# Kernel tuning notes

Measured on AMD Instinct MI355X. Metric: run time of the kernel, lower is better.

The kernel has to match this reference:

```python
import jax, jax.numpy as jnp
import numpy as np

HEADS = 16
D_MODEL = 1024
D_K = D_MODEL // HEADS
SEQ = 2048
BSZ = 2


def softmax_one(x, axis):
    # softmax with an extra +1 in the denominator ("attention off" slot)
    x = x - jnp.max(x, axis=axis, keepdims=True)
    ex = jnp.exp(x)
    return ex / (1.0 + jnp.sum(ex, axis=axis, keepdims=True))


def setup_inputs() -> dict:
    key = jax.random.key(0)
    ks = jax.random.split(key, 7)
    s = 1.0 / np.sqrt(D_MODEL)
    return {
        "x": jax.random.normal(ks[0], (SEQ, BSZ, D_MODEL), dtype=jnp.float32),
        "Wq": jax.random.normal(ks[1], (D_MODEL, D_MODEL), dtype=jnp.float32) * s,
        "bq": jnp.zeros((D_MODEL,), dtype=jnp.float32),
        "Wk": jax.random.normal(ks[2], (D_MODEL, D_MODEL), dtype=jnp.float32) * s,
        "bk": jnp.zeros((D_MODEL,), dtype=jnp.float32),
        "Wv": jax.random.normal(ks[3], (D_MODEL, D_MODEL), dtype=jnp.float32) * s,
        "bv": jnp.zeros((D_MODEL,), dtype=jnp.float32),
    }


def reference(x, Wq, bq, Wk, bk, Wv, bv):
    S, B, D = x.shape
    q = (x @ Wq.T + bq).reshape(S, B, HEADS, D_K)
    k = (x @ Wk.T + bk).reshape(S, B, HEADS, D_K)
    v = (x @ Wv.T + bv).reshape(S, B, HEADS, D_K)
    # [i, j, b, h] full score tensor, scaled by sqrt(d_k)
    scores = jnp.einsum('ibhd,jbhd->ijbh', q, k) / np.sqrt(D_K).astype(np.float32)
    causal = jnp.tril(jnp.ones((S, S), dtype=bool))[:, :, None, None]
    scores = jnp.where(causal, scores, -jnp.inf)
    attn = softmax_one(scores, axis=1)  # softmax over key axis j with +1 denom
    out = jnp.einsum('ijbh,jbhd->ibhd', attn, v)
    return out.reshape(S, B, D)
```

## Files before the change

### kernel.cpp

```cpp
#include <hip/hip_runtime.h>

#define SEQ 2048
#define BSZ 2
#define NH 16
#define DKD 64
#define DM 1024
#define NROW (SEQ*BSZ)
#define KDIM 1024
#define BIAS 16.0f

typedef __attribute__((ext_vector_type(8))) short bf16x8;
typedef __attribute__((ext_vector_type(4))) short bf16x4;
typedef __attribute__((ext_vector_type(4))) float floatx4;
typedef __attribute__((ext_vector_type(2))) unsigned uint2v;

__device__ __forceinline__ unsigned short f2b(float f) {
  unsigned int u = __builtin_bit_cast(unsigned int, f);
  u += 0x7fffu + ((u >> 16) & 1u);
  return (unsigned short)(u >> 16);
}

__device__ __forceinline__ void async_copy16(void* lds, const void* g) {
  __builtin_amdgcn_global_load_lds(
      (__attribute__((address_space(1))) void*)(void*)g,
      (__attribute__((address_space(3))) void*)lds, 16, 0, 0);
}

__device__ __forceinline__ floatx4 mfma16(bf16x8 a, bf16x8 b, floatx4 c) {
  return __builtin_amdgcn_mfma_f32_16x16x32_bf16(a, b, c, 0, 0, 0);
}

__device__ __forceinline__ floatx4 mfma16k(bf16x4 a, bf16x4 b, floatx4 c) {
#if __has_builtin(__builtin_amdgcn_mfma_f32_16x16x16bf16_1k)
  return __builtin_amdgcn_mfma_f32_16x16x16bf16_1k(a, b, c, 0, 0, 0);
#else
  floatx4 d;
  asm volatile("v_mfma_f32_16x16x16_bf16 %0, %1, %2, %3"
               : "=v"(d) : "v"(a), "v"(b), "v"(c));
  return d;
#endif
}

__global__ __launch_bounds__(256) void cvt_kernel(
    const float* __restrict__ x, const float* __restrict__ Wq,
    const float* __restrict__ Wk, const float* __restrict__ Wv,
    ushort* __restrict__ xbf, ushort* __restrict__ wbf) {
  size_t tid = (size_t)blockIdx.x * 256 + threadIdx.x;
  size_t i4 = tid * 4;
  const float* src;
  const size_t NX = (size_t)NROW * KDIM;
  ushort* dst;
  size_t off;
  if (i4 < NX) {
    src = x; off = i4; dst = xbf + i4;
  } else {
    size_t wix = i4 - NX;
    int proj = (int)(wix >> 20);
    src = proj == 0 ? Wq : (proj == 1 ? Wk : Wv);
    off = wix & 1048575u;
    dst = wbf + wix;
  }
  float4 v = *(const float4*)(src + off);
  ushort4 o;
  o.x = f2b(v.x); o.y = f2b(v.y); o.z = f2b(v.z); o.w = f2b(v.w);
  *(ushort4*)dst = o;
}

union GemmSmem {
  struct { ushort Al[128 * 32]; ushort Bl[128 * 32]; } ab;
  ushort Cl[128 * 136];
};

__global__ __launch_bounds__(256, 3) void gemm_qkv(
    const ushort* __restrict__ xbf, const ushort* __restrict__ wbf,
    const float* __restrict__ bq, const float* __restrict__ bk,
    const float* __restrict__ bvv,
    ushort* __restrict__ Qs, ushort* __restrict__ Ks, ushort* __restrict__ Vt) {
  __shared__ GemmSmem sm;
  const int t = threadIdx.x;
  const int w = t >> 6, l = t & 63;
  const int wr = w >> 1, wc = w & 1;
  const int lane15 = l & 15, quad = l >> 4;
  const int rb = blockIdx.x, cb = blockIdx.y;
  const ushort* Ag = xbf + (size_t)rb * 128 * KDIM;
  const ushort* Bg = wbf + (size_t)cb * 128 * KDIM;
  const int rsub = l >> 2, c2 = (l & 3) * 8;

  floatx4 acc[4][4];
  #pragma unroll
  for (int i = 0; i < 4; ++i)
    #pragma unroll
    for (int j = 0; j < 4; ++j) acc[i][j] = (floatx4){0.f, 0.f, 0.f, 0.f};

  for (int kk = 0; kk < KDIM; kk += 32) {
    __syncthreads();
    #pragma unroll
    for (int half = 0; half < 2; ++half) {
      int rloc = w * 32 + half * 16;
      async_copy16(&sm.ab.Al[rloc * 32], Ag + (size_t)(rloc + rsub) * KDIM + kk + c2);
      async_copy16(&sm.ab.Bl[rloc * 32], Bg + (size_t)(rloc + rsub) * KDIM + kk + c2);
    }
    __syncthreads();
    bf16x8 af[4], bfr[4];
    #pragma unroll
    for (int mt = 0; mt < 4; ++mt)
      af[mt] = *(const bf16x8*)&sm.ab.Al[(wr * 64 + mt * 16 + lane15) * 32 + quad * 8];
    #pragma unroll
    for (int nt = 0; nt < 4; ++nt)
      bfr[nt] = *(const bf16x8*)&sm.ab.Bl[(wc * 64 + nt * 16 + lane15) * 32 + quad * 8];
    #pragma unroll
    for (int mt = 0; mt < 4; ++mt)
      #pragma unroll
      for (int nt = 0; nt < 4; ++nt)
        acc[mt][nt] = mfma16(af[mt], bfr[nt], acc[mt][nt]);
  }
  __syncthreads();

  int proj = (cb * 128) >> 10;
  const float* bias = proj == 0 ? bq : (proj == 1 ? bk : bvv);
  float scale = proj == 0 ? 0.125f * 1.44269504088896f : 1.0f;
  bool isV = (proj == 2);

  #pragma unroll
  for (int nt = 0; nt < 4; ++nt) {
    int c = wc * 64 + nt * 16 + lane15;
    int cip = (cb * 128 + c) & 1023;
    float bias_v = bias[cip];
    #pragma unroll
    for (int mt = 0; mt < 4; ++mt) {
      #pragma unroll
      for (int r = 0; r < 4; ++r) {
        int n = wr * 64 + mt * 16 + quad * 4 + r;
        float val = (acc[mt][nt][r] + bias_v) * scale;
        if (!isV) sm.Cl[n * 136 + c] = f2b(val);
        else      sm.Cl[c * 136 + (n & 1) * 64 + (n >> 1)] = f2b(val);
      }
    }
  }
  __syncthreads();

  if (!isV) {
    ushort* dst = proj == 0 ? Qs : Ks;
    int b = t >> 7;
    int sl = t & 63;
    int chunk = (t >> 6) & 1;
    int n = (sl << 1) | b;
    int cip = (cb * 128 + chunk * 64) & 1023;
    int h = cip >> 6;
    int s = rb * 64 + sl;
    ushort* g = dst + (((size_t)(b * NH + h) * SEQ + s) * DKD);
    const uint4* s4 = (const uint4*)&sm.Cl[n * 136 + chunk * 64];
    #pragma unroll
    for (int j = 0; j < 8; ++j) *(uint4*)(g + j * 8) = s4[j];
  } else {
    int c = t >> 1, b = t & 1;
    int cip = (cb * 128 + c) & 1023;
    int h = cip >> 6, dk = c & 63;
    ushort* g = Vt + ((size_t)(b * NH + h) * DKD + dk) * SEQ + rb * 64;
    const uint4* s4 = (const uint4*)&sm.Cl[c * 136 + b * 64];
    #pragma unroll
    for (int j = 0; j < 8; ++j) *(uint4*)(g + j * 8) = s4[j];
  }
}

__global__ __launch_bounds__(256, 2) void attn_kernel(
    const ushort* __restrict__ Qs, const ushort* __restrict__ Ks,
    const ushort* __restrict__ Vt, float* __restrict__ out) {
  __shared__ ushort Kl[2][64 * 72];
  __shared__ ushort Vl[2][64 * 72];
  const int t = threadIdx.x;
  const int w = t >> 6, l = t & 63;
  const int lane15 = l & 15, quad = l >> 4;
  const int bh = blockIdx.x;
  const int qa = blockIdx.y;
  const int b = bh >> 4, h = bh & 15;

  const ushort* Kg = Ks + (size_t)bh * SEQ * DKD;
  const ushort* Vg = Vt + (size_t)bh * DKD * SEQ;
  const int srow = t >> 3;
  const int scol = (t & 7) * 8;

  int qt = qa;
  int qbase = qt * 64;
  const ushort* Qg = Qs + ((size_t)bh * SEQ + qbase + w * 16 + lane15) * DKD;
  bf16x8 qf0 = *(const bf16x8*)(Qg + quad * 8);
  bf16x8 qf1 = *(const bf16x8*)(Qg + 32 + quad * 8);

  floatx4 o[4];
  #pragma unroll
  for (int i = 0; i < 4; ++i) o[i] = (floatx4){0.f, 0.f, 0.f, 0.f};
  floatx4 lacc = (floatx4){0.f, 0.f, 0.f, 0.f};
  float pm = -1e30f;

  bf16x4 ones4;
  #pragma unroll
  for (int j = 0; j < 4; ++j) ones4[j] = (short)0x3F80;

  #define KT_OF(j) ((j) <= qa ? (j) : (j) - qa - 1)

  uint4 kr0, kr1, vr0, vr1;
  {
    kr0 = *(const uint4*)(Kg + (size_t)srow * DKD + scol);
    kr1 = *(const uint4*)(Kg + (size_t)(srow + 32) * DKD + scol);
    vr0 = *(const uint4*)(Vg + (size_t)srow * SEQ + scol);
    vr1 = *(const uint4*)(Vg + (size_t)(srow + 32) * SEQ + scol);
    *(uint4*)&Kl[0][srow * 72 + scol] = kr0;
    *(uint4*)&Kl[0][(srow + 32) * 72 + scol] = kr1;
    *(uint4*)&Vl[0][srow * 72 + scol] = vr0;
    *(uint4*)&Vl[0][(srow + 32) * 72 + scol] = vr1;
    int kt1 = KT_OF(1);
    kr0 = *(const uint4*)(Kg + (size_t)(kt1 * 64 + srow) * DKD + scol);
    kr1 = *(const uint4*)(Kg + (size_t)(kt1 * 64 + srow + 32) * DKD + scol);
    vr0 = *(const uint4*)(Vg + (size_t)srow * SEQ + kt1 * 64 + scol);
    vr1 = *(const uint4*)(Vg + (size_t)(srow + 32) * SEQ + kt1 * 64 + scol);
  }

  for (int it = 0; it <= 32; ++it) {
    const int cur = it & 1;
    const int kt = KT_OF(it);
    __syncthreads();

    floatx4 sf[4];
    #pragma unroll
    for (int nt = 0; nt < 4; ++nt) {
      floatx4 a = (floatx4){-BIAS, -BIAS, -BIAS, -BIAS};
      bf16x8 k0 = *(const bf16x8*)&Kl[cur][(nt * 16 + lane15) * 72 + quad * 8];
      bf16x8 k1 = *(const bf16x8*)&Kl[cur][(nt * 16 + lane15) * 72 + 32 + quad * 8];
      a = mfma16(k0, qf0, a);
      a = mfma16(k1, qf1, a);
      sf[nt] = a;
    }

    if (kt == qt) {
      int q_abs = qbase + w * 16 + lane15;
      #pragma unroll
      for (int nt = 0; nt < 4; ++nt) {
        #pragma unroll
        for (int r = 0; r < 4; ++r) {
          int k_abs = kt * 64 + nt * 16 + quad * 4 + r;
          if (k_abs > q_abs) sf[nt][r] = -1e30f;
        }
      }
    }

    bf16x4 pa[4];
    #pragma unroll
    for (int nt = 0; nt < 4; ++nt) {
      float p0 = __builtin_amdgcn_exp2f(sf[nt][0]);
      float p1 = __builtin_amdgcn_exp2f(sf[nt][1]);
      float p2 = __builtin_amdgcn_exp2f(sf[nt][2]);
      float p3 = __builtin_amdgcn_exp2f(sf[nt][3]);
      pm = fmaxf(pm, fmaxf(fmaxf(sf[nt][0], sf[nt][1]),
                           fmaxf(sf[nt][2], sf[nt][3])));
      unsigned u0 = __builtin_bit_cast(unsigned, p0);
      unsigned u1 = __builtin_bit_cast(unsigned, p1);
      unsigned u2 = __builtin_bit_cast(unsigned, p2);
      unsigned u3 = __builtin_bit_cast(unsigned, p3);
      uint2v pk;
      pk[0] = (u0 >> 16) | (u1 & 0xffff0000u);
      pk[1] = (u2 >> 16) | (u3 & 0xffff0000u);
      pa[nt] = __builtin_bit_cast(bf16x4, pk);
    }

    #pragma unroll
    for (int nt = 0; nt < 4; ++nt) lacc = mfma16k(pa[nt], ones4, lacc);
    #pragma unroll
    for (int ntd = 0; ntd < 4; ++ntd) {
      #pragma unroll
      for (int nt = 0; nt < 4; ++nt) {
        bf16x4 vf = *(const bf16x4*)&Vl[cur][(ntd * 16 + lane15) * 72 +
                                            nt * 16 + quad * 4];
        o[ntd] = mfma16k(pa[nt], vf, o[ntd]);
      }
    }

    if (it == qa || it == 32) {
      float pmr = fmaxf(pm, __shfl_xor(pm, 16, 64));
      pmr = fmaxf(pmr, __shfl_xor(pmr, 32, 64));
      float inv_[4];
      #pragma unroll
      for (int r = 0; r < 4; ++r) {
        float mq = __shfl(pmr, quad * 4 + r, 64);
        inv_[r] = 1.0f / (__builtin_amdgcn_exp2f(mq) + lacc[r]);
      }
      #pragma unroll
      for (int ntd = 0; ntd < 4; ++ntd) {
        int d = h * DKD + ntd * 16 + lane15;
        #pragma unroll
        for (int r = 0; r < 4; ++r) {
          int i = qbase + w * 16 + quad * 4 + r;
          out[((size_t)i * BSZ + b) * DM + d] = o[ntd][r] * inv_[r];
        }
      }
      if (it == qa) {
        #pragma unroll
        for (int i = 0; i < 4; ++i) o[i] = (floatx4){0.f, 0.f, 0.f, 0.f};
        lacc = (floatx4){0.f, 0.f, 0.f, 0.f};
        pm = -1e30f;
        qt = 31 - qa;
        qbase = qt * 64;
        const ushort* Qg2 = Qs + ((size_t)bh * SEQ + qbase + w * 16 + lane15) * DKD;
        qf0 = *(const bf16x8*)(Qg2 + quad * 8);
        qf1 = *(const bf16x8*)(Qg2 + 32 + quad * 8);
      }
    }

    if (it < 32) {
      int nxt = cur ^ 1;
      *(uint4*)&Kl[nxt][srow * 72 + scol] = kr0;
      *(uint4*)&Kl[nxt][(srow + 32) * 72 + scol] = kr1;
      *(uint4*)&Vl[nxt][srow * 72 + scol] = vr0;
      *(uint4*)&Vl[nxt][(srow + 32) * 72 + scol] = vr1;
      if (it + 2 <= 32) {
        int kt2 = KT_OF(it + 2);
        kr0 = *(const uint4*)(Kg + (size_t)(kt2 * 64 + srow) * DKD + scol);
        kr1 = *(const uint4*)(Kg + (size_t)(kt2 * 64 + srow + 32) * DKD + scol);
        vr0 = *(const uint4*)(Vg + (size_t)srow * SEQ + kt2 * 64 + scol);
        vr1 = *(const uint4*)(Vg + (size_t)(srow + 32) * SEQ + kt2 * 64 + scol);
      }
    }
  }
  #undef KT_OF
}

extern "C" void kernel_launch(void* const* d_in, const int* in_sizes, int n_in,
                              void* d_out, int out_size, void* d_ws, size_t ws_size,
                              hipStream_t stream) {
  (void)in_sizes; (void)n_in; (void)out_size; (void)ws_size;
  const float* x  = (const float*)d_in[0];
  const float* Wq = (const float*)d_in[1];
  const float* bq = (const float*)d_in[2];
  const float* Wk = (const float*)d_in[3];
  const float* bk = (const float*)d_in[4];
  const float* Wv = (const float*)d_in[5];
  const float* bv = (const float*)d_in[6];
  float* out = (float*)d_out;

  ushort* xbf = (ushort*)d_out;
  ushort* wbf = (ushort*)((char*)d_out + 8388608);

  char* ws = (char*)d_ws;
  ushort* Qs = (ushort*)(ws);
  ushort* Ks = (ushort*)(ws + 8388608);
  ushort* Vt = (ushort*)(ws + 16777216);

  cvt_kernel<<<dim3(7168), dim3(256), 0, stream>>>(x, Wq, Wk, Wv, xbf, wbf);
  gemm_qkv<<<dim3(32, 24), dim3(256), 0, stream>>>(xbf, wbf, bq, bk, bv, Qs, Ks, Vt);
  attn_kernel<<<dim3(32, 16), dim3(256), 0, stream>>>(Qs, Ks, Vt, out);
}
```

Baseline: 162.8 us.

## Double GEMM K-step with swizzled LDS and use 128-key tiles in attention

The QKV GEMM now stages 64-wide K slices per iteration, with an XOR swizzle on the LDS layout, so it needs half as many barriers and avoids bank conflicts on the fragment reads. The attention kernel loads 128-key K/V tiles per iteration, halving the loop count and its barriers, and skips the upper 64-key half on diagonal tiles. Each paired query tile now runs against 17 iterations of 128 keys instead of 33 of 64. LDS use roughly doubles in both kernels, which could lower occupancy, and the staged registers per thread also double.

```diff
diff --git a/kernel.cpp b/kernel.cpp
--- a/kernel.cpp
+++ b/kernel.cpp
@@ -67,7 +67,7 @@
 }
 
 union GemmSmem {
-  struct { ushort Al[128 * 32]; ushort Bl[128 * 32]; } ab;
+  struct { ushort Al[128 * 64]; ushort Bl[128 * 64]; } ab;
   ushort Cl[128 * 136];
 };
 
@@ -84,7 +84,8 @@
   const int rb = blockIdx.x, cb = blockIdx.y;
   const ushort* Ag = xbf + (size_t)rb * 128 * KDIM;
   const ushort* Bg = wbf + (size_t)cb * 128 * KDIM;
-  const int rsub = l >> 2, c2 = (l & 3) * 8;
+  const int srsub = l >> 3;
+  const int sgc = ((l & 7) ^ (l >> 3)) * 8;
 
   floatx4 acc[4][4];
   #pragma unroll
@@ -92,27 +93,40 @@
     #pragma unroll
     for (int j = 0; j < 4; ++j) acc[i][j] = (floatx4){0.f, 0.f, 0.f, 0.f};
 
-  for (int kk = 0; kk < KDIM; kk += 32) {
+  const int swzA = (lane15 & 7);
+
+  for (int kk = 0; kk < KDIM; kk += 64) {
     __syncthreads();
     #pragma unroll
-    for (int half = 0; half < 2; ++half) {
-      int rloc = w * 32 + half * 16;
-      async_copy16(&sm.ab.Al[rloc * 32], Ag + (size_t)(rloc + rsub) * KDIM + kk + c2);
-      async_copy16(&sm.ab.Bl[rloc * 32], Bg + (size_t)(rloc + rsub) * KDIM + kk + c2);
+    for (int c = 0; c < 4; ++c) {
+      int rloc = c * 32 + w * 8;
+      async_copy16(&sm.ab.Al[rloc * 64],
+                   Ag + (size_t)(rloc + srsub) * KDIM + kk + sgc);
+      async_copy16(&sm.ab.Bl[rloc * 64],
+                   Bg + (size_t)(rloc + srsub) * KDIM + kk + sgc);
     }
     __syncthreads();
-    bf16x8 af[4], bfr[4];
-    #pragma unroll
-    for (int mt = 0; mt < 4; ++mt)
-      af[mt] = *(const bf16x8*)&sm.ab.Al[(wr * 64 + mt * 16 + lane15) * 32 + quad * 8];
-    #pragma unroll
-    for (int nt = 0; nt < 4; ++nt)
-      bfr[nt] = *(const bf16x8*)&sm.ab.Bl[(wc * 64 + nt * 16 + lane15) * 32 + quad * 8];
-    #pragma unroll
-    for (int mt = 0; mt < 4; ++mt)
-      #pragma unroll
-      for (int nt = 0; nt < 4; ++nt)
-        acc[mt][nt] = mfma16(af[mt], bfr[nt], acc[mt][nt]);
+    #pragma unroll
+    for (int ks = 0; ks < 2; ++ks) {
+      bf16x8 af[4], bfr[4];
+      #pragma unroll
+      for (int mt = 0; mt < 4; ++mt) {
+        int row = wr * 64 + mt * 16 + lane15;
+        int pos = ((quad + ks * 4) ^ swzA) * 8;
+        af[mt] = *(const bf16x8*)&sm.ab.Al[row * 64 + pos];
+      }
+      #pragma unroll
+      for (int nt = 0; nt < 4; ++nt) {
+        int row = wc * 64 + nt * 16 + lane15;
+        int pos = ((quad + ks * 4) ^ swzA) * 8;
+        bfr[nt] = *(const bf16x8*)&sm.ab.Bl[row * 64 + pos];
+      }
+      #pragma unroll
+      for (int mt = 0; mt < 4; ++mt)
+        #pragma unroll
+        for (int nt = 0; nt < 4; ++nt)
+          acc[mt][nt] = mfma16(af[mt], bfr[nt], acc[mt][nt]);
+    }
   }
   __syncthreads();
 
@@ -166,19 +180,22 @@
 __global__ __launch_bounds__(256, 2) void attn_kernel(
     const ushort* __restrict__ Qs, const ushort* __restrict__ Ks,
     const ushort* __restrict__ Vt, float* __restrict__ out) {
-  __shared__ ushort Kl[2][64 * 72];
-  __shared__ ushort Vl[2][64 * 72];
+  __shared__ ushort Kl[2][128 * 72];
+  __shared__ ushort Vl[2][64 * 136];
   const int t = threadIdx.x;
   const int w = t >> 6, l = t & 63;
   const int lane15 = l & 15, quad = l >> 4;
   const int bh = blockIdx.x;
   const int qa = blockIdx.y;
   const int b = bh >> 4, h = bh & 15;
+  const int lastA = qa >> 1;
 
   const ushort* Kg = Ks + (size_t)bh * SEQ * DKD;
   const ushort* Vg = Vt + (size_t)bh * DKD * SEQ;
-  const int srow = t >> 3;
-  const int scol = (t & 7) * 8;
+  const int krow = t >> 3;
+  const int kcol = (t & 7) * 8;
+  const int vrow = t >> 4;
+  const int vcol = (t & 15) * 8;
 
   int qt = qa;
   int qbase = qt * 64;
@@ -196,85 +213,93 @@
   #pragma unroll
   for (int j = 0; j < 4; ++j) ones4[j] = (short)0x3F80;
 
-  #define KT_OF(j) ((j) <= qa ? (j) : (j) - qa - 1)
-
-  uint4 kr0, kr1, vr0, vr1;
-  {
-    kr0 = *(const uint4*)(Kg + (size_t)srow * DKD + scol);
-    kr1 = *(const uint4*)(Kg + (size_t)(srow + 32) * DKD + scol);
-    vr0 = *(const uint4*)(Vg + (size_t)srow * SEQ + scol);
-    vr1 = *(const uint4*)(Vg + (size_t)(srow + 32) * SEQ + scol);
-    *(uint4*)&Kl[0][srow * 72 + scol] = kr0;
-    *(uint4*)&Kl[0][(srow + 32) * 72 + scol] = kr1;
-    *(uint4*)&Vl[0][srow * 72 + scol] = vr0;
-    *(uint4*)&Vl[0][(srow + 32) * 72 + scol] = vr1;
-    int kt1 = KT_OF(1);
-    kr0 = *(const uint4*)(Kg + (size_t)(kt1 * 64 + srow) * DKD + scol);
-    kr1 = *(const uint4*)(Kg + (size_t)(kt1 * 64 + srow + 32) * DKD + scol);
-    vr0 = *(const uint4*)(Vg + (size_t)srow * SEQ + kt1 * 64 + scol);
-    vr1 = *(const uint4*)(Vg + (size_t)(srow + 32) * SEQ + kt1 * 64 + scol);
-  }
-
-  for (int it = 0; it <= 32; ++it) {
+  #define KT_OF(j) ((j) <= lastA ? (j) : (j) - lastA - 1)
+
+  uint4 kr[4], vr[4];
+  #define LOAD_G(KT) do {                                                    \
+    _Pragma("unroll")                                                        \
+    for (int c = 0; c < 4; ++c) {                                            \
+      kr[c] = *(const uint4*)(Kg + (size_t)((KT) * 128 + krow + c * 32) * DKD\
+                              + kcol);                                       \
+      vr[c] = *(const uint4*)(Vg + (size_t)(vrow + c * 16) * SEQ             \
+                              + (KT) * 128 + vcol);                          \
+    } } while (0)
+  #define STORE_L(BUF) do {                                                  \
+    _Pragma("unroll")                                                        \
+    for (int c = 0; c < 4; ++c) {                                            \
+      *(uint4*)&Kl[BUF][(krow + c * 32) * 72 + kcol] = kr[c];                \
+      *(uint4*)&Vl[BUF][(vrow + c * 16) * 136 + vcol] = vr[c];               \
+    } } while (0)
+
+  LOAD_G(0); STORE_L(0); LOAD_G(KT_OF(1));
+
+  for (int it = 0; it <= 16; ++it) {
     const int cur = it & 1;
     const int kt = KT_OF(it);
+    const bool edge = (it == lastA) || (it == 16);
     __syncthreads();
 
-    floatx4 sf[4];
-    #pragma unroll
-    for (int nt = 0; nt < 4; ++nt) {
-      floatx4 a = (floatx4){-BIAS, -BIAS, -BIAS, -BIAS};
-      bf16x8 k0 = *(const bf16x8*)&Kl[cur][(nt * 16 + lane15) * 72 + quad * 8];
-      bf16x8 k1 = *(const bf16x8*)&Kl[cur][(nt * 16 + lane15) * 72 + 32 + quad * 8];
-      a = mfma16(k0, qf0, a);
-      a = mfma16(k1, qf1, a);
-      sf[nt] = a;
-    }
-
-    if (kt == qt) {
-      int q_abs = qbase + w * 16 + lane15;
+    #pragma unroll
+    for (int kh = 0; kh < 2; ++kh) {
+      const int kb = kt * 128 + kh * 64;
+      if (edge && kb > qbase + 63) continue;
+
+      floatx4 sf[4];
       #pragma unroll
       for (int nt = 0; nt < 4; ++nt) {
-        #pragma unroll
-        for (int r = 0; r < 4; ++r) {
-          int k_abs = kt * 64 + nt * 16 + quad * 4 + r;
-          if (k_abs > q_abs) sf[nt][r] = -1e30f;
+        floatx4 a = (floatx4){-BIAS, -BIAS, -BIAS, -BIAS};
+        int row = kh * 64 + nt * 16 + lane15;
+        bf16x8 k0 = *(const bf16x8*)&Kl[cur][row * 72 + quad * 8];
+        bf16x8 k1 = *(const bf16x8*)&Kl[cur][row * 72 + 32 + quad * 8];
+        a = mfma16(k0, qf0, a);
+        a = mfma16(k1, qf1, a);
+        sf[nt] = a;
+      }
+
+      if (edge) {
+        int q_abs = qbase + w * 16 + lane15;
+        #pragma unroll
+        for (int nt = 0; nt < 4; ++nt)
+          #pragma unroll
+          for (int r = 0; r < 4; ++r) {
+            int k_abs = kb + nt * 16 + quad * 4 + r;
+            if (k_abs > q_abs) sf[nt][r] = -1e30f;
+          }
+      }
+
+      bf16x4 pa[4];
+      #pragma unroll
+      for (int nt = 0; nt < 4; ++nt) {
+        float p0 = __builtin_amdgcn_exp2f(sf[nt][0]);
+        float p1 = __builtin_amdgcn_exp2f(sf[nt][1]);
+        float p2 = __builtin_amdgcn_exp2f(sf[nt][2]);
+        float p3 = __builtin_amdgcn_exp2f(sf[nt][3]);
+        pm = fmaxf(pm, fmaxf(fmaxf(sf[nt][0], sf[nt][1]),
+                             fmaxf(sf[nt][2], sf[nt][3])));
+        unsigned u0 = __builtin_bit_cast(unsigned, p0);
+        unsigned u1 = __builtin_bit_cast(unsigned, p1);
+        unsigned u2 = __builtin_bit_cast(unsigned, p2);
+        unsigned u3 = __builtin_bit_cast(unsigned, p3);
+        uint2v pk;
+        pk[0] = (u0 >> 16) | (u1 & 0xffff0000u);
+        pk[1] = (u2 >> 16) | (u3 & 0xffff0000u);
+        pa[nt] = __builtin_bit_cast(bf16x4, pk);
+      }
+
+      #pragma unroll
+      for (int nt = 0; nt < 4; ++nt) lacc = mfma16k(pa[nt], ones4, lacc);
+      #pragma unroll
+      for (int ntd = 0; ntd < 4; ++ntd) {
+        #pragma unroll
+        for (int nt = 0; nt < 4; ++nt) {
+          bf16x4 vf = *(const bf16x4*)&Vl[cur][(ntd * 16 + lane15) * 136 +
+                                              kh * 64 + nt * 16 + quad * 4];
+          o[ntd] = mfma16k(pa[nt], vf, o[ntd]);
         }
       }
     }
 
-    bf16x4 pa[4];
-    #pragma unroll
-    for (int nt = 0; nt < 4; ++nt) {
-      float p0 = __builtin_amdgcn_exp2f(sf[nt][0]);
-      float p1 = __builtin_amdgcn_exp2f(sf[nt][1]);
-      float p2 = __builtin_amdgcn_exp2f(sf[nt][2]);
-      float p3 = __builtin_amdgcn_exp2f(sf[nt][3]);
-      pm = fmaxf(pm, fmaxf(fmaxf(sf[nt][0], sf[nt][1]),
-                           fmaxf(sf[nt][2], sf[nt][3])));
-      unsigned u0 = __builtin_bit_cast(unsigned, p0);
-      unsigned u1 = __builtin_bit_cast(unsigned, p1);
-      unsigned u2 = __builtin_bit_cast(unsigned, p2);
-      unsigned u3 = __builtin_bit_cast(unsigned, p3);
-      uint2v pk;
-      pk[0] = (u0 >> 16) | (u1 & 0xffff0000u);
-      pk[1] = (u2 >> 16) | (u3 & 0xffff0000u);
-      pa[nt] = __builtin_bit_cast(bf16x4, pk);
-    }
-
-    #pragma unroll
-    for (int nt = 0; nt < 4; ++nt) lacc = mfma16k(pa[nt], ones4, lacc);
-    #pragma unroll
-    for (int ntd = 0; ntd < 4; ++ntd) {
-      #pragma unroll
-      for (int nt = 0; nt < 4; ++nt) {
-        bf16x4 vf = *(const bf16x4*)&Vl[cur][(ntd * 16 + lane15) * 72 +
-                                            nt * 16 + quad * 4];
-        o[ntd] = mfma16k(pa[nt], vf, o[ntd]);
-      }
-    }
-
-    if (it == qa || it == 32) {
+    if (edge) {
       float pmr = fmaxf(pm, __shfl_xor(pm, 16, 64));
       pmr = fmaxf(pmr, __shfl_xor(pmr, 32, 64));
       float inv_[4];
@@ -292,7 +317,7 @@
           out[((size_t)i * BSZ + b) * DM + d] = o[ntd][r] * inv_[r];
         }
       }
-      if (it == qa) {
+      if (it == lastA) {
         #pragma unroll
         for (int i = 0; i < 4; ++i) o[i] = (floatx4){0.f, 0.f, 0.f, 0.f};
         lacc = (floatx4){0.f, 0.f, 0.f, 0.f};
@@ -305,21 +330,13 @@
       }
     }
 
-    if (it < 32) {
-      int nxt = cur ^ 1;
-      *(uint4*)&Kl[nxt][srow * 72 + scol] = kr0;
-      *(uint4*)&Kl[nxt][(srow + 32) * 72 + scol] = kr1;
-      *(uint4*)&Vl[nxt][srow * 72 + scol] = vr0;
-      *(uint4*)&Vl[nxt][(srow + 32) * 72 + scol] = vr1;
-      if (it + 2 <= 32) {
-        int kt2 = KT_OF(it + 2);
-        kr0 = *(const uint4*)(Kg + (size_t)(kt2 * 64 + srow) * DKD + scol);
-        kr1 = *(const uint4*)(Kg + (size_t)(kt2 * 64 + srow + 32) * DKD + scol);
-        vr0 = *(const uint4*)(Vg + (size_t)srow * SEQ + kt2 * 64 + scol);
-        vr1 = *(const uint4*)(Vg + (size_t)(srow + 32) * SEQ + kt2 * 64 + scol);
-      }
-    }
-  }
+    if (it < 16) {
+      STORE_L(cur ^ 1);
+      if (it + 2 <= 16) LOAD_G(KT_OF(it + 2));
+    }
+  }
+  #undef STORE_L
+  #undef LOAD_G
   #undef KT_OF
 }
 
```

Result: slower. 211.4 us (+29.8%).

## Stage K/V tiles via async global-to-LDS copies with XOR-swizzled layout

Applied to the files above, without the earlier changes.

Replaces the register-staged K/V prefetch (global load to registers, then store to LDS) with direct global_load_lds async copies into the next buffer, issued right after the barrier. The LDS layout drops the 72-element padding in favour of an XOR swizzle on 16-byte chunks, which keeps bank conflicts low for the fragment reads. This frees registers and removes the LDS store instructions, but it depends on the async copy finishing before the next barrier. The prefetch distance shrinks from two tiles ahead to one.

```diff
diff --git a/kernel.cpp b/kernel.cpp
--- a/kernel.cpp
+++ b/kernel.cpp
@@ -166,8 +166,8 @@
 __global__ __launch_bounds__(256, 2) void attn_kernel(
     const ushort* __restrict__ Qs, const ushort* __restrict__ Ks,
     const ushort* __restrict__ Vt, float* __restrict__ out) {
-  __shared__ ushort Kl[2][64 * 72];
-  __shared__ ushort Vl[2][64 * 72];
+  __shared__ ushort Kl[2][64 * 64];
+  __shared__ ushort Vl[2][64 * 64];
   const int t = threadIdx.x;
   const int w = t >> 6, l = t & 63;
   const int lane15 = l & 15, quad = l >> 4;
@@ -177,8 +177,9 @@
 
   const ushort* Kg = Ks + (size_t)bh * SEQ * DKD;
   const ushort* Vg = Vt + (size_t)bh * DKD * SEQ;
-  const int srow = t >> 3;
-  const int scol = (t & 7) * 8;
+  const int g8 = l >> 3;
+  const int gch = ((l & 7) ^ g8) * 8;
+  const int sw = lane15 & 7;
 
   int qt = qa;
   int qbase = qt * 64;
@@ -198,34 +199,31 @@
 
   #define KT_OF(j) ((j) <= qa ? (j) : (j) - qa - 1)
 
-  uint4 kr0, kr1, vr0, vr1;
-  {
-    kr0 = *(const uint4*)(Kg + (size_t)srow * DKD + scol);
-    kr1 = *(const uint4*)(Kg + (size_t)(srow + 32) * DKD + scol);
-    vr0 = *(const uint4*)(Vg + (size_t)srow * SEQ + scol);
-    vr1 = *(const uint4*)(Vg + (size_t)(srow + 32) * SEQ + scol);
-    *(uint4*)&Kl[0][srow * 72 + scol] = kr0;
-    *(uint4*)&Kl[0][(srow + 32) * 72 + scol] = kr1;
-    *(uint4*)&Vl[0][srow * 72 + scol] = vr0;
-    *(uint4*)&Vl[0][(srow + 32) * 72 + scol] = vr1;
-    int kt1 = KT_OF(1);
-    kr0 = *(const uint4*)(Kg + (size_t)(kt1 * 64 + srow) * DKD + scol);
-    kr1 = *(const uint4*)(Kg + (size_t)(kt1 * 64 + srow + 32) * DKD + scol);
-    vr0 = *(const uint4*)(Vg + (size_t)srow * SEQ + kt1 * 64 + scol);
-    vr1 = *(const uint4*)(Vg + (size_t)(srow + 32) * SEQ + kt1 * 64 + scol);
-  }
+  #define STAGE(BUF, KT) do {                                                \
+    _Pragma("unroll")                                                        \
+    for (int c = 0; c < 2; ++c) {                                            \
+      int rr = w * 16 + c * 8;                                               \
+      async_copy16(&Kl[BUF][rr * 64],                                        \
+                   Kg + (size_t)((KT) * 64 + rr + g8) * DKD + gch);          \
+      async_copy16(&Vl[BUF][rr * 64],                                        \
+                   Vg + (size_t)(rr + g8) * SEQ + (KT) * 64 + gch);          \
+    } } while (0)
+
+  STAGE(0, 0);
 
   for (int it = 0; it <= 32; ++it) {
     const int cur = it & 1;
     const int kt = KT_OF(it);
     __syncthreads();
+    if (it < 32) STAGE(cur ^ 1, KT_OF(it + 1));
 
     floatx4 sf[4];
     #pragma unroll
     for (int nt = 0; nt < 4; ++nt) {
       floatx4 a = (floatx4){-BIAS, -BIAS, -BIAS, -BIAS};
-      bf16x8 k0 = *(const bf16x8*)&Kl[cur][(nt * 16 + lane15) * 72 + quad * 8];
-      bf16x8 k1 = *(const bf16x8*)&Kl[cur][(nt * 16 + lane15) * 72 + 32 + quad * 8];
+      int row = nt * 16 + lane15;
+      bf16x8 k0 = *(const bf16x8*)&Kl[cur][row * 64 + ((quad ^ sw) * 8)];
+      bf16x8 k1 = *(const bf16x8*)&Kl[cur][row * 64 + (((quad + 4) ^ sw) * 8)];
       a = mfma16(k0, qf0, a);
       a = mfma16(k1, qf1, a);
       sf[nt] = a;
@@ -234,13 +232,12 @@
     if (kt == qt) {
       int q_abs = qbase + w * 16 + lane15;
       #pragma unroll
-      for (int nt = 0; nt < 4; ++nt) {
+      for (int nt = 0; nt < 4; ++nt)
         #pragma unroll
         for (int r = 0; r < 4; ++r) {
           int k_abs = kt * 64 + nt * 16 + quad * 4 + r;
           if (k_abs > q_abs) sf[nt][r] = -1e30f;
         }
-      }
     }
 
     bf16x4 pa[4];
@@ -266,10 +263,12 @@
     for (int nt = 0; nt < 4; ++nt) lacc = mfma16k(pa[nt], ones4, lacc);
     #pragma unroll
     for (int ntd = 0; ntd < 4; ++ntd) {
+      int row = ntd * 16 + lane15;
       #pragma unroll
       for (int nt = 0; nt < 4; ++nt) {
-        bf16x4 vf = *(const bf16x4*)&Vl[cur][(ntd * 16 + lane15) * 72 +
-                                            nt * 16 + quad * 4];
+        int ch = nt * 2 + (quad >> 1);
+        bf16x4 vf = *(const bf16x4*)&Vl[cur][row * 64 + ((ch ^ sw) * 8) +
+                                            (quad & 1) * 4];
         o[ntd] = mfma16k(pa[nt], vf, o[ntd]);
       }
     }
@@ -304,22 +303,8 @@
         qf1 = *(const bf16x8*)(Qg2 + 32 + quad * 8);
       }
     }
-
-    if (it < 32) {
-      int nxt = cur ^ 1;
-      *(uint4*)&Kl[nxt][srow * 72 + scol] = kr0;
-      *(uint4*)&Kl[nxt][(srow + 32) * 72 + scol] = kr1;
-      *(uint4*)&Vl[nxt][srow * 72 + scol] = vr0;
-      *(uint4*)&Vl[nxt][(srow + 32) * 72 + scol] = vr1;
-      if (it + 2 <= 32) {
-        int kt2 = KT_OF(it + 2);
-        kr0 = *(const uint4*)(Kg + (size_t)(kt2 * 64 + srow) * DKD + scol);
-        kr1 = *(const uint4*)(Kg + (size_t)(kt2 * 64 + srow + 32) * DKD + scol);
-        vr0 = *(const uint4*)(Vg + (size_t)srow * SEQ + kt2 * 64 + scol);
-        vr1 = *(const uint4*)(Vg + (size_t)(srow + 32) * SEQ + kt2 * 64 + scol);
-      }
-    }
-  }
+  }
+  #undef STAGE
   #undef KT_OF
 }
 
```

New measurement: 164.3 us. Within noise of the previous version (+0.9%).
